# Performance work log

Measured on AMD Instinct MI355X. Metric: run time of the kernel, lower is better.

The kernel has to match this reference:

```python
import jax, jax.numpy as jnp
import numpy as np
from jax import lax

# --- Haar (db1) wavelet filters, per WTConv (dec filters use reversed pywt taps) ---
_R = 0.7071067811865476
_lo = jnp.array([_R, _R], jnp.float32)
_hi = jnp.array([_R, -_R], jnp.float32)
# order: LL, (hi rows)x(lo cols), (lo rows)x(hi cols), HH  — matches WTConv stack order
DEC = jnp.stack([_lo[:, None] * _lo[None, :], _hi[:, None] * _lo[None, :],
                 _lo[:, None] * _hi[None, :], _hi[:, None] * _hi[None, :]])  # [4,2,2]
REC = DEC  # Haar is orthogonal: rec filters equal dec filters


def dwconv(x, w):
    # depthwise conv, SAME padding; x [b,c,h,w], w [c,1,kh,kw]
    return lax.conv_general_dilated(x, w, (1, 1), 'SAME',
                                    feature_group_count=x.shape[1],
                                    dimension_numbers=('NCHW', 'OIHW', 'NCHW'))


def wtconv(x, base_w, base_s, wav_w, wav_s):
    # WTConv2d, wt_levels=1, Haar: base depthwise path + wavelet-domain depthwise conv path
    b, c, h, w = x.shape
    # analysis: stride-2 2x2 filters == non-overlapping block contraction
    s = jnp.einsum('bchpwq,fpq->bcfhw', x.reshape(b, c, h // 2, 2, w // 2, 2), DEC)
    s = s.reshape(b, 4 * c, h // 2, w // 2)
    s = dwconv(s, wav_w) * wav_s[None, :, None, None]  # conv subbands + scale (init 0.1)
    # synthesis: transposed stride-2 conv == block expansion
    y = jnp.einsum('bcfhw,fpq->bchpwq', s.reshape(b, c, 4, h // 2, w // 2), REC)
    y = y.reshape(b, c, h, w)
    return dwconv(x, base_w) * base_s[None, :, None, None] + y


def _forward(x, crossFeat, Wq, Wk, Wv, temperature,
             qdw_base_w, qdw_base_s, qdw_wav_w, qdw_wav_s,
             kdw_base_w, kdw_base_s, kdw_wav_w, kdw_wav_s,
             vdw_base_w, vdw_base_s, vdw_wav_w, vdw_wav_s,
             proj_base_w, proj_base_s, proj_wav_w, proj_wav_s):
    heads = temperature.shape[0]
    b, _, H, W = crossFeat.shape
    q = jnp.einsum('bchw,oc->bohw', x, Wq)          # 1x1 conv, bias=False
    k = jnp.einsum('bchw,oc->bohw', crossFeat, Wk)
    v = jnp.einsum('bchw,oc->bohw', crossFeat, Wv)
    q = wtconv(q, qdw_base_w, qdw_base_s, qdw_wav_w, qdw_wav_s)
    k = wtconv(k, kdw_base_w, kdw_base_s, kdw_wav_w, kdw_wav_s)
    v = wtconv(v, vdw_base_w, vdw_base_s, vdw_wav_w, vdw_wav_s)
    dim = q.shape[1]
    # F.interpolate(mode='bilinear', align_corners=False) == jax.image.resize 'bilinear'
    q = jax.image.resize(q, (b, dim, H, W), 'bilinear')
    ch = dim // heads
    q = q.reshape(b, heads, ch, H * W)
    k = k.reshape(b, heads, ch, H * W)
    v = v.reshape(b, heads, ch, H * W)
    # L2-normalize along spatial dim (torch F.normalize eps=1e-12)
    q = q / jnp.maximum(jnp.linalg.norm(q, axis=-1, keepdims=True), 1e-12)
    k = k / jnp.maximum(jnp.linalg.norm(k, axis=-1, keepdims=True), 1e-12)
    attn = jnp.einsum('bhcn,bhdn->bhcd', q, k) * temperature[None]  # [b,h,ch,ch]
    attn = jax.nn.softmax(attn, axis=-1)
    out = jnp.einsum('bhcd,bhdn->bhcn', attn, v).reshape(b, dim, H, W)
    return wtconv(out, proj_base_w, proj_base_s, proj_wav_w, proj_wav_s)


def setup_inputs() -> dict:
    key = jax.random.key(0)
    ks = iter(jax.random.split(key, 32))
    B, CIN, DIM, HEADS = 2, 256, 256, 8
    d = {}
    d['x'] = jax.random.normal(next(ks), (B, CIN, 64, 64), jnp.float32)
    d['crossFeat'] = jax.random.normal(next(ks), (B, CIN, 128, 128), jnp.float32)
    d['Wq'] = jax.random.normal(next(ks), (DIM, CIN), jnp.float32) * 0.05
    d['Wk'] = jax.random.normal(next(ks), (DIM, CIN), jnp.float32) * 0.05
    d['Wv'] = jax.random.normal(next(ks), (DIM, CIN), jnp.float32) * 0.05
    d['temperature'] = jnp.ones((HEADS, 1, 1), jnp.float32)
    for pre, ksz in [('qdw', 3), ('kdw', 3), ('vdw', 3), ('proj', 1)]:
        d[pre + '_base_w'] = jax.random.normal(next(ks), (DIM, 1, ksz, ksz), jnp.float32) * 0.1
        d[pre + '_base_s'] = jnp.ones((DIM,), jnp.float32)
        d[pre + '_wav_w'] = jax.random.normal(next(ks), (4 * DIM, 1, ksz, ksz), jnp.float32) * 0.1
        d[pre + '_wav_s'] = 0.1 * jnp.ones((4 * DIM,), jnp.float32)
    return d


def reference(x, crossFeat, Wq, Wk, Wv, temperature,
              qdw_base_w, qdw_base_s, qdw_wav_w, qdw_wav_s,
              kdw_base_w, kdw_base_s, kdw_wav_w, kdw_wav_s,
              vdw_base_w, vdw_base_s, vdw_wav_w, vdw_wav_s,
              proj_base_w, proj_base_s, proj_wav_w, proj_wav_s):
    return _forward(x, crossFeat, Wq, Wk, Wv, temperature,
                    qdw_base_w, qdw_base_s, qdw_wav_w, qdw_wav_s,
                    kdw_base_w, kdw_base_s, kdw_wav_w, kdw_wav_s,
                    vdw_base_w, vdw_base_s, vdw_wav_w, vdw_wav_s,
                    proj_base_w, proj_base_s, proj_wav_w, proj_wav_s)
```

## Files before the change

kernel.cpp:

```cpp
#include <hip/hip_runtime.h>
#include <math.h>

constexpr int B_ = 2;
constexpr int C_ = 256;
constexpr int Hb_ = 128, Wb_ = 128;
constexpr int Nb_ = Hb_ * Wb_;
constexpr int Hs_ = 64, Ws_ = 64;
constexpr int Ns_ = Hs_ * Ws_;
constexpr int HEADS_ = 8;
constexpr int CHD_ = C_ / HEADS_;

typedef float f32x4 __attribute__((ext_vector_type(4)));

template<int NTOT>
__global__ __launch_bounds__(256) void gemm_1x1(const float* __restrict__ in,
                                                const float* __restrict__ Wm,
                                                float* __restrict__ out) {
  constexpr int BK = 32;
  __shared__ float Wsh[BK][68];
  __shared__ float Xsh[BK][128];
  const int b  = blockIdx.z;
  const int o0 = blockIdx.y * 64;
  const int n0 = blockIdx.x * 128;
  const float* inb = in + (size_t)b * C_ * NTOT;
  const int t  = threadIdx.x;
  const int ty = t >> 4, tx = t & 15;
  float acc[4][8] = {};
  for (int k0 = 0; k0 < C_; k0 += BK) {
    {
      int oo = t & 63, kb = (t >> 6) << 3;
      const float* wp = Wm + (size_t)(o0 + oo) * C_ + k0 + kb;
      float4 w0 = *(const float4*)wp;
      float4 w1 = *(const float4*)(wp + 4);
      Wsh[kb + 0][oo] = w0.x; Wsh[kb + 1][oo] = w0.y;
      Wsh[kb + 2][oo] = w0.z; Wsh[kb + 3][oo] = w0.w;
      Wsh[kb + 4][oo] = w1.x; Wsh[kb + 5][oo] = w1.y;
      Wsh[kb + 6][oo] = w1.z; Wsh[kb + 7][oo] = w1.w;
    }
    {
      int nn = (t & 31) << 2;
      int kr0 = t >> 5;
#pragma unroll
      for (int r = 0; r < 4; ++r) {
        int kr = kr0 + r * 8;
        *(float4*)&Xsh[kr][nn] = *(const float4*)(inb + (size_t)(k0 + kr) * NTOT + n0 + nn);
      }
    }
    __syncthreads();
#pragma unroll
    for (int kk = 0; kk < BK; ++kk) {
      float4 af = *(float4*)&Wsh[kk][ty * 4];
      float4 x0 = *(float4*)&Xsh[kk][tx * 4];
      float4 x1 = *(float4*)&Xsh[kk][tx * 4 + 64];
      float av[4] = {af.x, af.y, af.z, af.w};
      float xv[8] = {x0.x, x0.y, x0.z, x0.w, x1.x, x1.y, x1.z, x1.w};
#pragma unroll
      for (int i = 0; i < 4; ++i)
#pragma unroll
        for (int j = 0; j < 8; ++j)
          acc[i][j] = fmaf(av[i], xv[j], acc[i][j]);
    }
    __syncthreads();
  }
  float* ob = out + (size_t)b * C_ * NTOT;
#pragma unroll
  for (int i = 0; i < 4; ++i) {
    float* op = ob + (size_t)(o0 + ty * 4 + i) * NTOT + n0;
    *(float4*)(op + tx * 4)      = make_float4(acc[i][0], acc[i][1], acc[i][2], acc[i][3]);
    *(float4*)(op + tx * 4 + 64) = make_float4(acc[i][4], acc[i][5], acc[i][6], acc[i][7]);
  }
}

__global__ __launch_bounds__(256) void gemm_dual(const float* __restrict__ in,
                                                 const float* __restrict__ Wk,
                                                 const float* __restrict__ Wv,
                                                 float* __restrict__ outK,
                                                 float* __restrict__ outV) {
  constexpr int BK = 32;
  constexpr int NTOT = Nb_;
  __shared__ float WshK[BK][68];
  __shared__ float WshV[BK][68];
  __shared__ float Xsh[BK][128];
  const int b  = blockIdx.z;
  const int o0 = blockIdx.y * 64;
  const int n0 = blockIdx.x * 128;
  const float* inb = in + (size_t)b * C_ * NTOT;
  const int t  = threadIdx.x;
  const int ty = t >> 4, tx = t & 15;
  float accK[4][8] = {}, accV[4][8] = {};
  const int oo = t & 63, kb = (t >> 6) << 3;
  for (int k0 = 0; k0 < C_; k0 += BK) {
    {
      const float* wp = Wk + (size_t)(o0 + oo) * C_ + k0 + kb;
      float4 w0 = *(const float4*)wp;
      float4 w1 = *(const float4*)(wp + 4);
      WshK[kb + 0][oo] = w0.x; WshK[kb + 1][oo] = w0.y;
      WshK[kb + 2][oo] = w0.z; WshK[kb + 3][oo] = w0.w;
      WshK[kb + 4][oo] = w1.x; WshK[kb + 5][oo] = w1.y;
      WshK[kb + 6][oo] = w1.z; WshK[kb + 7][oo] = w1.w;
    }
    {
      const float* wp = Wv + (size_t)(o0 + oo) * C_ + k0 + kb;
      float4 w0 = *(const float4*)wp;
      float4 w1 = *(const float4*)(wp + 4);
      WshV[kb + 0][oo] = w0.x; WshV[kb + 1][oo] = w0.y;
      WshV[kb + 2][oo] = w0.z; WshV[kb + 3][oo] = w0.w;
      WshV[kb + 4][oo] = w1.x; WshV[kb + 5][oo] = w1.y;
      WshV[kb + 6][oo] = w1.z; WshV[kb + 7][oo] = w1.w;
    }
    {
      int nn = (t & 31) << 2;
      int kr0 = t >> 5;
#pragma unroll
      for (int r = 0; r < 4; ++r) {
        int kr = kr0 + r * 8;
        *(float4*)&Xsh[kr][nn] = *(const float4*)(inb + (size_t)(k0 + kr) * NTOT + n0 + nn);
      }
    }
    __syncthreads();
#pragma unroll
    for (int kk = 0; kk < BK; ++kk) {
      float4 ak = *(float4*)&WshK[kk][ty * 4];
      float4 avv = *(float4*)&WshV[kk][ty * 4];
      float4 x0 = *(float4*)&Xsh[kk][tx * 4];
      float4 x1 = *(float4*)&Xsh[kk][tx * 4 + 64];
      float akv[4] = {ak.x, ak.y, ak.z, ak.w};
      float avv4[4] = {avv.x, avv.y, avv.z, avv.w};
      float xv[8] = {x0.x, x0.y, x0.z, x0.w, x1.x, x1.y, x1.z, x1.w};
#pragma unroll
      for (int i = 0; i < 4; ++i)
#pragma unroll
        for (int j = 0; j < 8; ++j) {
          accK[i][j] = fmaf(akv[i], xv[j], accK[i][j]);
          accV[i][j] = fmaf(avv4[i], xv[j], accV[i][j]);
        }
    }
    __syncthreads();
  }
  float* obK = outK + (size_t)b * C_ * NTOT;
  float* obV = outV + (size_t)b * C_ * NTOT;
#pragma unroll
  for (int i = 0; i < 4; ++i) {
    size_t ro = (size_t)(o0 + ty * 4 + i) * NTOT + n0;
    *(float4*)(obK + ro + tx * 4)      = make_float4(accK[i][0], accK[i][1], accK[i][2], accK[i][3]);
    *(float4*)(obK + ro + tx * 4 + 64) = make_float4(accK[i][4], accK[i][5], accK[i][6], accK[i][7]);
    *(float4*)(obV + ro + tx * 4)      = make_float4(accV[i][0], accV[i][1], accV[i][2], accV[i][3]);
    *(float4*)(obV + ro + tx * 4 + 64) = make_float4(accV[i][4], accV[i][5], accV[i][6], accV[i][7]);
  }
}

template<int HP>
__global__ __launch_bounds__(256) void wtconv_fused(
    const float* __restrict__ x, const float* __restrict__ bw,
    const float* __restrict__ bs, const float* __restrict__ ww,
    const float* __restrict__ wsc, float* __restrict__ out,
    float* __restrict__ nrm) {
  constexpr int NT = HP / 64;
  const int tile = blockIdx.x;
  const int c = blockIdx.y, b = blockIdx.z;
  const int oy = (tile / NT) * 64, ox = (tile % NT) * 64;
  const float* xp = x + ((size_t)(b * C_) + c) * HP * HP;

  __shared__ float xt[68][76];
  __shared__ f32x4 sb4[34][36];
  __shared__ float red[4];

  float wb[9];
#pragma unroll
  for (int i = 0; i < 9; ++i) wb[i] = bw[c * 9 + i];
  const float sbase = bs[c];
  f32x4 wv4[9]; f32x4 sv4;
#pragma unroll
  for (int i = 0; i < 9; ++i) {
    wv4[i].x = ww[(c * 4 + 0) * 9 + i];
    wv4[i].y = ww[(c * 4 + 1) * 9 + i];
    wv4[i].z = ww[(c * 4 + 2) * 9 + i];
    wv4[i].w = ww[(c * 4 + 3) * 9 + i];
  }
  sv4.x = wsc[c * 4 + 0]; sv4.y = wsc[c * 4 + 1];
  sv4.z = wsc[c * 4 + 2]; sv4.w = wsc[c * 4 + 3];

  const int t = threadIdx.x;
  for (int p = t; p < 68 * 18; p += 256) {
    int r = p / 18, k4 = (p % 18) << 2;
    int gy = oy - 2 + r, gx = ox - 4 + k4;
    float4 v = make_float4(0.f, 0.f, 0.f, 0.f);
    if ((unsigned)gy < (unsigned)HP && (unsigned)gx < (unsigned)HP)
      v = *(const float4*)(xp + (size_t)gy * HP + gx);
    *(float4*)&xt[r][k4] = v;
  }
  __syncthreads();
  for (int p = t; p < 34 * 34; p += 256) {
    int i = p / 34, j = p % 34;
    float p00 = xt[2 * i][2 * j + 2],     p01 = xt[2 * i][2 * j + 3];
    float p10 = xt[2 * i + 1][2 * j + 2], p11 = xt[2 * i + 1][2 * j + 3];
    f32x4 s;
    s.x = 0.5f * (p00 + p01 + p10 + p11);
    s.y = 0.5f * (p00 + p01 - p10 - p11);
    s.z = 0.5f * (p00 - p01 + p10 - p11);
    s.w = 0.5f * (p00 - p01 - p10 + p11);
    sb4[i][j] = s;
  }
  __syncthreads();

  float nacc = 0.f;
  float* op0 = out + ((size_t)(b * C_) + c) * HP * HP;
  for (int p = t; p < 32 * 32; p += 256) {
    int i = p >> 5, j = p & 31;
    f32x4 a4 = {0.f, 0.f, 0.f, 0.f};
#pragma unroll
    for (int dh = 0; dh < 3; ++dh)
#pragma unroll
      for (int dw = 0; dw < 3; ++dw)
        a4 += sb4[i + dh][j + dw] * wv4[dh * 3 + dw];
    f32x4 s4 = a4 * sv4;
    float pp[4][4];
#pragma unroll
    for (int r = 0; r < 4; ++r)
#pragma unroll
      for (int cc = 0; cc < 4; ++cc)
        pp[r][cc] = xt[2 * i + 1 + r][2 * j + 3 + cc];
    float o4[2][2];
#pragma unroll
    for (int di = 0; di < 2; ++di)
#pragma unroll
      for (int dj = 0; dj < 2; ++dj) {
        float a = 0.f;
#pragma unroll
        for (int dh = 0; dh < 3; ++dh)
#pragma unroll
          for (int dw = 0; dw < 3; ++dw)
            a = fmaf(pp[di + dh][dj + dw], wb[dh * 3 + dw], a);
        a *= sbase;
        float s1 = di ? -s4.y : s4.y;
        float s2 = dj ? -s4.z : s4.z;
        float s3 = (di ^ dj) ? -s4.w : s4.w;
        o4[di][dj] = a + 0.5f * (s4.x + s1 + s2 + s3);
      }
    float* op = op0 + (size_t)(oy + 2 * i) * HP + ox + 2 * j;
    *(float2*)op        = make_float2(o4[0][0], o4[0][1]);
    *(float2*)(op + HP) = make_float2(o4[1][0], o4[1][1]);
    nacc += o4[0][0] * o4[0][0] + o4[0][1] * o4[0][1] +
            o4[1][0] * o4[1][0] + o4[1][1] * o4[1][1];
  }
  if (nrm != nullptr) {
#pragma unroll
    for (int m = 32; m; m >>= 1) nacc += __shfl_xor(nacc, m, 64);
    int lane = t & 63, wv_ = t >> 6;
    if (lane == 0) red[wv_] = nacc;
    __syncthreads();
    if (t == 0)
      atomicAdd(&nrm[b * C_ + c], red[0] + red[1] + red[2] + red[3]);
  }
}

__global__ __launch_bounds__(256) void resize2x_norm(const float* __restrict__ in,
                                                     float* __restrict__ out,
                                                     float* __restrict__ rnq_sum) {
  const int bc = blockIdx.x;
  const int t = threadIdx.x;
  __shared__ float xs[64][65];
  __shared__ float red[4];
  const float* ip = in + (size_t)bc * Ns_;
  for (int p = t; p < 1024; p += 256) {
    float4 v = *(const float4*)&ip[p << 2];
    int r = p >> 4, c0 = (p & 15) << 2;
    xs[r][c0] = v.x; xs[r][c0 + 1] = v.y; xs[r][c0 + 2] = v.z; xs[r][c0 + 3] = v.w;
  }
  __syncthreads();
  float* op = out + (size_t)bc * Nb_;
  float nacc = 0.f;
#pragma unroll
  for (int it = 0; it < 16; ++it) {
    int p = t + it * 256;
    int i = p >> 5;
    int jc = p & 31;
    int ti = i >> 1; bool oi = i & 1;
    int r0 = oi ? ti : (ti > 0 ? ti - 1 : 0);
    int r1 = oi ? (ti < 63 ? ti + 1 : 63) : ti;
    float wr0 = oi ? 0.75f : 0.25f, wr1 = oi ? 0.25f : 0.75f;
    int cb = jc << 1;
    int cm1 = cb > 0 ? cb - 1 : 0;
    int cp2 = cb < 62 ? cb + 2 : 63;
    float a0 = xs[r0][cm1], a1 = xs[r0][cb], a2 = xs[r0][cb + 1], a3 = xs[r0][cp2];
    float b0 = xs[r1][cm1], b1 = xs[r1][cb], b2 = xs[r1][cb + 1], b3 = xs[r1][cp2];
    float ha0 = 0.25f * a0 + 0.75f * a1, hb0 = 0.25f * b0 + 0.75f * b1;
    float ha1 = 0.75f * a1 + 0.25f * a2, hb1 = 0.75f * b1 + 0.25f * b2;
    float ha2 = 0.25f * a1 + 0.75f * a2, hb2 = 0.25f * b1 + 0.75f * b2;
    float ha3 = 0.75f * a2 + 0.25f * a3, hb3 = 0.75f * b2 + 0.25f * b3;
    float4 o = make_float4(wr0 * ha0 + wr1 * hb0, wr0 * ha1 + wr1 * hb1,
                           wr0 * ha2 + wr1 * hb2, wr0 * ha3 + wr1 * hb3);
    *(float4*)&op[p << 2] = o;
    nacc += o.x * o.x + o.y * o.y + o.z * o.z + o.w * o.w;
  }
#pragma unroll
  for (int m = 32; m; m >>= 1) nacc += __shfl_xor(nacc, m, 64);
  int lane = t & 63, wv = t >> 6;
  if (lane == 0) red[wv] = nacc;
  __syncthreads();
  if (t == 0) rnq_sum[bc] = red[0] + red[1] + red[2] + red[3];
}

__global__ void zero_buf(float* __restrict__ p, int n) {
  int i = blockIdx.x * blockDim.x + threadIdx.x;
  if (i < n) p[i] = 0.f;
}

__global__ __launch_bounds__(256) void gram_qk(const float* __restrict__ q,
                                               const float* __restrict__ k,
                                               float* __restrict__ gram) {
  const int b = blockIdx.z, h = blockIdx.y, sl = blockIdx.x;
  constexpr int NS = Nb_ / 32;
  const int n0 = sl * NS;
  const int t = threadIdx.x;
  const int tc = t >> 4, td = t & 15;
  const float* qb = q + ((size_t)b * C_ + h * CHD_) * Nb_;
  const float* kb = k + ((size_t)b * C_ + h * CHD_) * Nb_;
  __shared__ float qs[32][132];
  __shared__ float kst[128][34];
  float a00 = 0.f, a01 = 0.f, a10 = 0.f, a11 = 0.f;
  for (int nc = 0; nc < NS; nc += 128) {
    for (int i = t; i < 1024; i += 256) {
      int row = i >> 5, nc4 = (i & 31) << 2;
      float4 qv = *(const float4*)&qb[(size_t)row * Nb_ + n0 + nc + nc4];
      *(float4*)&qs[row][nc4] = qv;
      float4 kv = *(const float4*)&kb[(size_t)row * Nb_ + n0 + nc + nc4];
      kst[nc4 + 0][row] = kv.x; kst[nc4 + 1][row] = kv.y;
      kst[nc4 + 2][row] = kv.z; kst[nc4 + 3][row] = kv.w;
    }
    __syncthreads();
#pragma unroll 8
    for (int nn = 0; nn < 128; ++nn) {
      float q0 = qs[2 * tc][nn], q1 = qs[2 * tc + 1][nn];
      float2 kk = *(float2*)&kst[nn][2 * td];
      a00 = fmaf(q0, kk.x, a00); a01 = fmaf(q0, kk.y, a01);
      a10 = fmaf(q1, kk.x, a10); a11 = fmaf(q1, kk.y, a11);
    }
    __syncthreads();
  }
  float* gp = gram + ((size_t)(b * HEADS_ + h) * CHD_ + 2 * tc) * CHD_ + 2 * td;
  atomicAdd(&gp[0], a00);
  atomicAdd(&gp[1], a01);
  atomicAdd(&gp[CHD_], a10);
  atomicAdd(&gp[CHD_ + 1], a11);
}

__global__ __launch_bounds__(1024) void attn_softmax(const float* __restrict__ gram,
                                                     const float* __restrict__ rnq_sum,
                                                     const float* __restrict__ rnk_sum,
                                                     const float* __restrict__ temp,
                                                     float* __restrict__ attn) {
  const int h = blockIdx.x, b = blockIdx.y;
  const int t = threadIdx.x;
  const int c = t >> 5, d = t & 31;
  size_t gi = ((size_t)(b * HEADS_ + h) * CHD_ + c) * CHD_ + d;
  float rq = 1.f / fmaxf(sqrtf(rnq_sum[b * C_ + h * CHD_ + c]), 1e-12f);
  float rk = 1.f / fmaxf(sqrtf(rnk_sum[b * C_ + h * CHD_ + d]), 1e-12f);
  float val = gram[gi] * rq * rk * temp[h];
  float m = val;
#pragma unroll
  for (int s = 16; s; s >>= 1) m = fmaxf(m, __shfl_xor(m, s, 64));
  float e = expf(val - m);
  float ssum = e;
#pragma unroll
  for (int s = 16; s; s >>= 1) ssum += __shfl_xor(ssum, s, 64);
  attn[gi] = e / ssum;
}

__global__ __launch_bounds__(256) void av_proj(const float* __restrict__ attn,
                                               const float* __restrict__ v,
                                               const float* __restrict__ p_bw,
                                               const float* __restrict__ p_bs,
                                               const float* __restrict__ p_ww,
                                               const float* __restrict__ p_ws,
                                               float* __restrict__ out) {
  const int bh = blockIdx.y;
  const int b = bh >> 3, h = bh & 7;
  const int half = threadIdx.x >> 7;
  const int pl = threadIdx.x & 127;
  const int p = blockIdx.x * 128 + pl;
  const int bi = p >> 6, bj = p & 63;
  __shared__ float at[32][36];
  for (int i = threadIdx.x; i < 1024; i += 256)
    at[i & 31][i >> 5] = attn[(size_t)bh * 1024 + i];
  __syncthreads();
  const float* vb = v + ((size_t)b * C_ + h * CHD_) * Nb_;
  const int n00 = (2 * bi) * Wb_ + 2 * bj;
  float acc[16][4] = {};
  for (int d = 0; d < 32; ++d) {
    const float* vp = vb + (size_t)d * Nb_ + n00;
    float2 vt = *(const float2*)vp;
    float2 vbt = *(const float2*)(vp + Wb_);
    float4 a0 = *(float4*)&at[d][half * 16];
    float4 a1 = *(float4*)&at[d][half * 16 + 4];
    float4 a2 = *(float4*)&at[d][half * 16 + 8];
    float4 a3 = *(float4*)&at[d][half * 16 + 12];
    float av[16] = {a0.x, a0.y, a0.z, a0.w, a1.x, a1.y, a1.z, a1.w,
                    a2.x, a2.y, a2.z, a2.w, a3.x, a3.y, a3.z, a3.w};
#pragma unroll
    for (int cc = 0; cc < 16; ++cc) {
      acc[cc][0] = fmaf(av[cc], vt.x,  acc[cc][0]);
      acc[cc][1] = fmaf(av[cc], vt.y,  acc[cc][1]);
      acc[cc][2] = fmaf(av[cc], vbt.x, acc[cc][2]);
      acc[cc][3] = fmaf(av[cc], vbt.y, acc[cc][3]);
    }
  }
  float* ob = out + ((size_t)b * C_ + h * CHD_) * Nb_;
#pragma unroll
  for (int cc = 0; cc < 16; ++cc) {
    int lc = half * 16 + cc;
    int gc = h * CHD_ + lc;
    float p00 = acc[cc][0], p01 = acc[cc][1], p10 = acc[cc][2], p11 = acc[cc][3];
    float ll = 0.5f * (p00 + p01 + p10 + p11) * (p_ww[gc * 4 + 0] * p_ws[gc * 4 + 0]);
    float hl = 0.5f * (p00 + p01 - p10 - p11) * (p_ww[gc * 4 + 1] * p_ws[gc * 4 + 1]);
    float lh = 0.5f * (p00 - p01 + p10 - p11) * (p_ww[gc * 4 + 2] * p_ws[gc * 4 + 2]);
    float hh = 0.5f * (p00 - p01 - p10 + p11) * (p_ww[gc * 4 + 3] * p_ws[gc * 4 + 3]);
    float bb = p_bw[gc] * p_bs[gc];
    float* op = ob + (size_t)lc * Nb_ + n00;
    *(float2*)op         = make_float2(p00 * bb + 0.5f * (ll + hl + lh + hh),
                                       p01 * bb + 0.5f * (ll + hl - lh - hh));
    *(float2*)(op + Wb_) = make_float2(p10 * bb + 0.5f * (ll - hl + lh - hh),
                                       p11 * bb + 0.5f * (ll - hl - lh + hh));
  }
}

extern "C" void kernel_launch(void* const* d_in, const int* in_sizes, int n_in,
                              void* d_out, int out_size, void* d_ws, size_t ws_size,
                              hipStream_t stream) {
  const float* x    = (const float*)d_in[0];
  const float* cf   = (const float*)d_in[1];
  const float* Wq   = (const float*)d_in[2];
  const float* Wk   = (const float*)d_in[3];
  const float* Wv   = (const float*)d_in[4];
  const float* temp = (const float*)d_in[5];
  const float* q_bw = (const float*)d_in[6];
  const float* q_bs = (const float*)d_in[7];
  const float* q_ww = (const float*)d_in[8];
  const float* q_ws = (const float*)d_in[9];
  const float* k_bw = (const float*)d_in[10];
  const float* k_bs = (const float*)d_in[11];
  const float* k_ww = (const float*)d_in[12];
  const float* k_ws = (const float*)d_in[13];
  const float* v_bw = (const float*)d_in[14];
  const float* v_bs = (const float*)d_in[15];
  const float* v_ww = (const float*)d_in[16];
  const float* v_ws = (const float*)d_in[17];
  const float* p_bw = (const float*)d_in[18];
  const float* p_bs = (const float*)d_in[19];
  const float* p_ww = (const float*)d_in[20];
  const float* p_ws = (const float*)d_in[21];

  float* ws   = (float*)d_ws;
  float* A    = ws;
  float* Bb   = A  + 2097152;
  float* Cb   = Bb + 8388608;
  float* Fb   = Cb + 8388608;
  float* Gb   = Fb + 2097152;
  float* Hb   = Gb + 8388608;
  float* rnq  = Hb + 8388608;
  float* rnk  = rnq + 512;
  float* gram = rnk + 512;
  float* attn = gram + 16384;

  zero_buf<<<(16896 + 255) / 256, 256, 0, stream>>>(rnk, 16896);

  gemm_1x1<Ns_><<<dim3(Ns_ / 128, C_ / 64, B_), 256, 0, stream>>>(x, Wq, A);
  gemm_dual<<<dim3(Nb_ / 128, C_ / 64, B_), 256, 0, stream>>>(cf, Wk, Wv, Bb, Cb);

  wtconv_fused<64><<<dim3(1, C_, B_), 256, 0, stream>>>(A, q_bw, q_bs, q_ww, q_ws, Fb, nullptr);
  wtconv_fused<128><<<dim3(4, C_, B_), 256, 0, stream>>>(Bb, k_bw, k_bs, k_ww, k_ws, Gb, rnk);
  wtconv_fused<128><<<dim3(4, C_, B_), 256, 0, stream>>>(Cb, v_bw, v_bs, v_ww, v_ws, Hb, nullptr);

  resize2x_norm<<<B_ * C_, 256, 0, stream>>>(Fb, Bb, rnq);

  gram_qk<<<dim3(32, HEADS_, B_), 256, 0, stream>>>(Bb, Gb, gram);
  attn_softmax<<<dim3(HEADS_, B_), 1024, 0, stream>>>(gram, rnq, rnk, temp, attn);

  av_proj<<<dim3(Nb_ / 4 / 128, B_ * HEADS_), 256, 0, stream>>>(
      attn, Hb, p_bw, p_bs, p_ww, p_ws, (float*)d_out);
}
```

Measured before the change: 340.9 us.

## Replace FP32 1x1-conv GEMMs with split-bf16 MFMA GEMMs on transposed inputs

The fp32 SIMT GEMMs for the Q/K/V 1x1 projections are replaced by bf16 MFMA GEMMs. Each fp32 value is split into high and low bf16 parts, and three MFMAs per product (hh, hl, lh) keep near-fp32 accuracy. New pre-pass kernels transpose the activations to channel-contiguous layout while splitting them, and split the weights. The extra conversion passes add memory traffic and workspace, and the output stores are scattered scalar writes.

New measurement: 286.6 us. -15.9%, faster.

```diff
diff --git a/kernel.cpp b/kernel.cpp
--- a/kernel.cpp
+++ b/kernel.cpp
@@ -11,141 +11,130 @@
 constexpr int CHD_ = C_ / HEADS_;
 
 typedef float f32x4 __attribute__((ext_vector_type(4)));
-
-template<int NTOT>
-__global__ __launch_bounds__(256) void gemm_1x1(const float* __restrict__ in,
-                                                const float* __restrict__ Wm,
-                                                float* __restrict__ out) {
-  constexpr int BK = 32;
-  __shared__ float Wsh[BK][68];
-  __shared__ float Xsh[BK][128];
+typedef short bf16x8 __attribute__((ext_vector_type(8)));
+typedef unsigned short u16x8 __attribute__((ext_vector_type(8)));
+
+__device__ inline void cvt_split(float f, unsigned short& h, unsigned short& l) {
+  unsigned u = __float_as_uint(f);
+  unsigned r = u + 0x7fffu + ((u >> 16) & 1u);
+  h = (unsigned short)(r >> 16);
+  float hf = __uint_as_float((unsigned)h << 16);
+  float lo = f - hf;
+  unsigned u2 = __float_as_uint(lo);
+  unsigned r2 = u2 + 0x7fffu + ((u2 >> 16) & 1u);
+  l = (unsigned short)(r2 >> 16);
+}
+
+__global__ __launch_bounds__(256) void cvt_split_T(const float* __restrict__ X,
+                                                   unsigned short* __restrict__ Xh,
+                                                   unsigned short* __restrict__ Xl,
+                                                   int NTOT) {
+  __shared__ float xs[64][72];
+  const int b  = blockIdx.z;
+  const int c0 = blockIdx.y * 64;
+  const int n0 = blockIdx.x * 64;
+  const int t  = threadIdx.x;
+  const float* xb = X + ((size_t)(b * C_ + c0)) * NTOT + n0;
+  {
+    int cl = t >> 4, n4 = (t & 15) << 2;
+#pragma unroll
+    for (int i = 0; i < 4; ++i) {
+      float4 v = *(const float4*)(xb + (size_t)(cl + 16 * i) * NTOT + n4);
+      *(float4*)&xs[cl + 16 * i][n4] = v;
+    }
+  }
+  __syncthreads();
+  const int n_l = t >> 2, cqb = t & 3;
+  size_t obase = ((size_t)b * NTOT + n0 + n_l) * C_ + c0;
+#pragma unroll
+  for (int it = 0; it < 2; ++it) {
+    int cq = it * 4 + cqb;
+    u16x8 hv, lv;
+#pragma unroll
+    for (int j = 0; j < 8; ++j) {
+      unsigned short h, l;
+      cvt_split(xs[cq * 8 + j][n_l], h, l);
+      hv[j] = h; lv[j] = l;
+    }
+    *(u16x8*)(Xh + obase + cq * 8) = hv;
+    *(u16x8*)(Xl + obase + cq * 8) = lv;
+  }
+}
+
+__global__ void cvt_w(const float* __restrict__ Wq, const float* __restrict__ Wk,
+                      const float* __restrict__ Wv, unsigned short* __restrict__ Wp) {
+  int i = blockIdx.x * 256 + threadIdx.x;
+  int m = i >> 16, idx = i & 65535;
+  const float* src = (m == 0) ? Wq : (m == 1) ? Wk : Wv;
+  unsigned short h, l;
+  cvt_split(src[idx], h, l);
+  Wp[(size_t)m * 131072 + idx] = h;
+  Wp[(size_t)m * 131072 + 65536 + idx] = l;
+}
+
+template<bool DUAL>
+__global__ __launch_bounds__(256) void gemm_mfma(
+    const unsigned short* __restrict__ XhT, const unsigned short* __restrict__ XlT,
+    const unsigned short* __restrict__ Wh1, const unsigned short* __restrict__ Wl1,
+    const unsigned short* __restrict__ Wh2, const unsigned short* __restrict__ Wl2,
+    float* __restrict__ out1, float* __restrict__ out2, int NTOT) {
+  __shared__ __align__(16) unsigned short XhL[64][40];
+  __shared__ __align__(16) unsigned short XlL[64][40];
   const int b  = blockIdx.z;
   const int o0 = blockIdx.y * 64;
-  const int n0 = blockIdx.x * 128;
-  const float* inb = in + (size_t)b * C_ * NTOT;
+  const int n0 = blockIdx.x * 64;
   const int t  = threadIdx.x;
-  const int ty = t >> 4, tx = t & 15;
-  float acc[4][8] = {};
-  for (int k0 = 0; k0 < C_; k0 += BK) {
+  const int w = t >> 6, lane = t & 63;
+  const int lr = lane & 15, lk = lane >> 4;
+  const unsigned short* xh = XhT + ((size_t)b * NTOT + n0) * C_;
+  const unsigned short* xl = XlT + ((size_t)b * NTOT + n0) * C_;
+  const int arow = o0 + w * 16 + lr;
+  f32x4 acc1[4] = {};
+  f32x4 acc2[4] = {};
+  const int sn = t >> 2, scq = (t & 3) << 3;
+  for (int c0 = 0; c0 < C_; c0 += 32) {
     {
-      int oo = t & 63, kb = (t >> 6) << 3;
-      const float* wp = Wm + (size_t)(o0 + oo) * C_ + k0 + kb;
-      float4 w0 = *(const float4*)wp;
-      float4 w1 = *(const float4*)(wp + 4);
-      Wsh[kb + 0][oo] = w0.x; Wsh[kb + 1][oo] = w0.y;
-      Wsh[kb + 2][oo] = w0.z; Wsh[kb + 3][oo] = w0.w;
-      Wsh[kb + 4][oo] = w1.x; Wsh[kb + 5][oo] = w1.y;
-      Wsh[kb + 6][oo] = w1.z; Wsh[kb + 7][oo] = w1.w;
-    }
-    {
-      int nn = (t & 31) << 2;
-      int kr0 = t >> 5;
-#pragma unroll
-      for (int r = 0; r < 4; ++r) {
-        int kr = kr0 + r * 8;
-        *(float4*)&Xsh[kr][nn] = *(const float4*)(inb + (size_t)(k0 + kr) * NTOT + n0 + nn);
+      size_t off = (size_t)sn * C_ + c0 + scq;
+      *(u16x8*)&XhL[sn][scq] = *(const u16x8*)(xh + off);
+      *(u16x8*)&XlL[sn][scq] = *(const u16x8*)(xl + off);
+    }
+    size_t aoff = (size_t)arow * C_ + c0 + lk * 8;
+    bf16x8 a1h = *(const bf16x8*)(Wh1 + aoff);
+    bf16x8 a1l = *(const bf16x8*)(Wl1 + aoff);
+    bf16x8 a2h, a2l;
+    if constexpr (DUAL) {
+      a2h = *(const bf16x8*)(Wh2 + aoff);
+      a2l = *(const bf16x8*)(Wl2 + aoff);
+    }
+    __syncthreads();
+#pragma unroll
+    for (int s = 0; s < 4; ++s) {
+      bf16x8 bh = *(const bf16x8*)&XhL[s * 16 + lr][lk * 8];
+      bf16x8 bl = *(const bf16x8*)&XlL[s * 16 + lr][lk * 8];
+      acc1[s] = __builtin_amdgcn_mfma_f32_16x16x32_bf16(a1h, bh, acc1[s], 0, 0, 0);
+      acc1[s] = __builtin_amdgcn_mfma_f32_16x16x32_bf16(a1h, bl, acc1[s], 0, 0, 0);
+      acc1[s] = __builtin_amdgcn_mfma_f32_16x16x32_bf16(a1l, bh, acc1[s], 0, 0, 0);
+      if constexpr (DUAL) {
+        acc2[s] = __builtin_amdgcn_mfma_f32_16x16x32_bf16(a2h, bh, acc2[s], 0, 0, 0);
+        acc2[s] = __builtin_amdgcn_mfma_f32_16x16x32_bf16(a2h, bl, acc2[s], 0, 0, 0);
+        acc2[s] = __builtin_amdgcn_mfma_f32_16x16x32_bf16(a2l, bh, acc2[s], 0, 0, 0);
       }
     }
     __syncthreads();
-#pragma unroll
-    for (int kk = 0; kk < BK; ++kk) {
-      float4 af = *(float4*)&Wsh[kk][ty * 4];
-      float4 x0 = *(float4*)&Xsh[kk][tx * 4];
-      float4 x1 = *(float4*)&Xsh[kk][tx * 4 + 64];
-      float av[4] = {af.x, af.y, af.z, af.w};
-      float xv[8] = {x0.x, x0.y, x0.z, x0.w, x1.x, x1.y, x1.z, x1.w};
-#pragma unroll
-      for (int i = 0; i < 4; ++i)
-#pragma unroll
-        for (int j = 0; j < 8; ++j)
-          acc[i][j] = fmaf(av[i], xv[j], acc[i][j]);
-    }
-    __syncthreads();
-  }
-  float* ob = out + (size_t)b * C_ * NTOT;
-#pragma unroll
-  for (int i = 0; i < 4; ++i) {
-    float* op = ob + (size_t)(o0 + ty * 4 + i) * NTOT + n0;
-    *(float4*)(op + tx * 4)      = make_float4(acc[i][0], acc[i][1], acc[i][2], acc[i][3]);
-    *(float4*)(op + tx * 4 + 64) = make_float4(acc[i][4], acc[i][5], acc[i][6], acc[i][7]);
-  }
-}
-
-__global__ __launch_bounds__(256) void gemm_dual(const float* __restrict__ in,
-                                                 const float* __restrict__ Wk,
-                                                 const float* __restrict__ Wv,
-                                                 float* __restrict__ outK,
-                                                 float* __restrict__ outV) {
-  constexpr int BK = 32;
-  constexpr int NTOT = Nb_;
-  __shared__ float WshK[BK][68];
-  __shared__ float WshV[BK][68];
-  __shared__ float Xsh[BK][128];
-  const int b  = blockIdx.z;
-  const int o0 = blockIdx.y * 64;
-  const int n0 = blockIdx.x * 128;
-  const float* inb = in + (size_t)b * C_ * NTOT;
-  const int t  = threadIdx.x;
-  const int ty = t >> 4, tx = t & 15;
-  float accK[4][8] = {}, accV[4][8] = {};
-  const int oo = t & 63, kb = (t >> 6) << 3;
-  for (int k0 = 0; k0 < C_; k0 += BK) {
-    {
-      const float* wp = Wk + (size_t)(o0 + oo) * C_ + k0 + kb;
-      float4 w0 = *(const float4*)wp;
-      float4 w1 = *(const float4*)(wp + 4);
-      WshK[kb + 0][oo] = w0.x; WshK[kb + 1][oo] = w0.y;
-      WshK[kb + 2][oo] = w0.z; WshK[kb + 3][oo] = w0.w;
-      WshK[kb + 4][oo] = w1.x; WshK[kb + 5][oo] = w1.y;
-      WshK[kb + 6][oo] = w1.z; WshK[kb + 7][oo] = w1.w;
-    }
-    {
-      const float* wp = Wv + (size_t)(o0 + oo) * C_ + k0 + kb;
-      float4 w0 = *(const float4*)wp;
-      float4 w1 = *(const float4*)(wp + 4);
-      WshV[kb + 0][oo] = w0.x; WshV[kb + 1][oo] = w0.y;
-      WshV[kb + 2][oo] = w0.z; WshV[kb + 3][oo] = w0.w;
-      WshV[kb + 4][oo] = w1.x; WshV[kb + 5][oo] = w1.y;
-      WshV[kb + 6][oo] = w1.z; WshV[kb + 7][oo] = w1.w;
-    }
-    {
-      int nn = (t & 31) << 2;
-      int kr0 = t >> 5;
-#pragma unroll
-      for (int r = 0; r < 4; ++r) {
-        int kr = kr0 + r * 8;
-        *(float4*)&Xsh[kr][nn] = *(const float4*)(inb + (size_t)(k0 + kr) * NTOT + n0 + nn);
-      }
-    }
-    __syncthreads();
-#pragma unroll
-    for (int kk = 0; kk < BK; ++kk) {
-      float4 ak = *(float4*)&WshK[kk][ty * 4];
-      float4 avv = *(float4*)&WshV[kk][ty * 4];
-      float4 x0 = *(float4*)&Xsh[kk][tx * 4];
-      float4 x1 = *(float4*)&Xsh[kk][tx * 4 + 64];
-      float akv[4] = {ak.x, ak.y, ak.z, ak.w};
-      float avv4[4] = {avv.x, avv.y, avv.z, avv.w};
-      float xv[8] = {x0.x, x0.y, x0.z, x0.w, x1.x, x1.y, x1.z, x1.w};
-#pragma unroll
-      for (int i = 0; i < 4; ++i)
-#pragma unroll
-        for (int j = 0; j < 8; ++j) {
-          accK[i][j] = fmaf(akv[i], xv[j], accK[i][j]);
-          accV[i][j] = fmaf(avv4[i], xv[j], accV[i][j]);
-        }
-    }
-    __syncthreads();
-  }
-  float* obK = outK + (size_t)b * C_ * NTOT;
-  float* obV = outV + (size_t)b * C_ * NTOT;
-#pragma unroll
-  for (int i = 0; i < 4; ++i) {
-    size_t ro = (size_t)(o0 + ty * 4 + i) * NTOT + n0;
-    *(float4*)(obK + ro + tx * 4)      = make_float4(accK[i][0], accK[i][1], accK[i][2], accK[i][3]);
-    *(float4*)(obK + ro + tx * 4 + 64) = make_float4(accK[i][4], accK[i][5], accK[i][6], accK[i][7]);
-    *(float4*)(obV + ro + tx * 4)      = make_float4(accV[i][0], accV[i][1], accV[i][2], accV[i][3]);
-    *(float4*)(obV + ro + tx * 4 + 64) = make_float4(accV[i][4], accV[i][5], accV[i][6], accV[i][7]);
+  }
+  float* o1 = out1 + ((size_t)(b * C_ + o0 + w * 16)) * NTOT + n0;
+#pragma unroll
+  for (int s = 0; s < 4; ++s)
+#pragma unroll
+    for (int r = 0; r < 4; ++r)
+      o1[(size_t)(lk * 4 + r) * NTOT + s * 16 + lr] = acc1[s][r];
+  if constexpr (DUAL) {
+    float* o2 = out2 + ((size_t)(b * C_ + o0 + w * 16)) * NTOT + n0;
+#pragma unroll
+    for (int s = 0; s < 4; ++s)
+#pragma unroll
+      for (int r = 0; r < 4; ++r)
+        o2[(size_t)(lk * 4 + r) * NTOT + s * 16 + lr] = acc2[s][r];
   }
 }
 
@@ -457,15 +446,31 @@
   float* Fb   = Cb + 8388608;
   float* Gb   = Fb + 2097152;
   float* Hb   = Gb + 8388608;
-  float* rnq  = Hb + 8388608;
+  float* XhKf = Hb + 8388608;
+  float* XlKf = XhKf + 4194304;
+  float* Xhxf = XlKf + 4194304;
+  float* Xlxf = Xhxf + 1048576;
+  float* Wpf  = Xlxf + 1048576;
+  float* rnq  = Wpf + 196608;
   float* rnk  = rnq + 512;
   float* gram = rnk + 512;
   float* attn = gram + 16384;
+  unsigned short* XhK = (unsigned short*)XhKf;
+  unsigned short* XlK = (unsigned short*)XlKf;
+  unsigned short* Xhx = (unsigned short*)Xhxf;
+  unsigned short* Xlx = (unsigned short*)Xlxf;
+  unsigned short* Wp  = (unsigned short*)Wpf;
 
   zero_buf<<<(16896 + 255) / 256, 256, 0, stream>>>(rnk, 16896);
 
-  gemm_1x1<Ns_><<<dim3(Ns_ / 128, C_ / 64, B_), 256, 0, stream>>>(x, Wq, A);
-  gemm_dual<<<dim3(Nb_ / 128, C_ / 64, B_), 256, 0, stream>>>(cf, Wk, Wv, Bb, Cb);
+  cvt_split_T<<<dim3(Nb_ / 64, C_ / 64, B_), 256, 0, stream>>>(cf, XhK, XlK, Nb_);
+  cvt_split_T<<<dim3(Ns_ / 64, C_ / 64, B_), 256, 0, stream>>>(x,  Xhx, Xlx, Ns_);
+  cvt_w<<<3 * 65536 / 256, 256, 0, stream>>>(Wq, Wk, Wv, Wp);
+
+  gemm_mfma<false><<<dim3(Ns_ / 64, C_ / 64, B_), 256, 0, stream>>>(
+      Xhx, Xlx, Wp, Wp + 65536, nullptr, nullptr, A, nullptr, Ns_);
+  gemm_mfma<true><<<dim3(Nb_ / 64, C_ / 64, B_), 256, 0, stream>>>(
+      XhK, XlK, Wp + 131072, Wp + 196608, Wp + 262144, Wp + 327680, Bb, Cb, Nb_);
 
   wtconv_fused<64><<<dim3(1, C_, B_), 256, 0, stream>>>(A, q_bw, q_bs, q_ww, q_ws, Fb, nullptr);
   wtconv_fused<128><<<dim3(4, C_, B_), 256, 0, stream>>>(Bb, k_bw, k_bs, k_ww, k_ws, Gb, rnk);
```
